# Kernel optimization log

Hardware: AMD Instinct MI355X
Metric: run time of the kernel (lower is better)

## Reference

```python
import jax, jax.numpy as jnp
import numpy as np

K = 16        # top-K nodes per sample (from self.K)
C_IN = 2048   # conv1 in_channels
C_OUT = 256   # conv1 out_channels
D_OUT = 512   # fc1 out_features (in_features = K*C_OUT = 4096)


def setup_inputs() -> dict:
    key = jax.random.key(0)
    k0, k1, k2 = jax.random.split(key, 3)
    N, W, H = 128, 16, 16
    sounds = jax.random.normal(k0, (N, C_IN, W, H), dtype=jnp.float32)
    conv_w = jax.random.normal(k1, (C_OUT, C_IN), dtype=jnp.float32) * 0.02
    conv_b = jnp.zeros((C_OUT,), jnp.float32)
    fc_w = jax.random.normal(k2, (D_OUT, K * C_OUT), dtype=jnp.float32) * 0.02
    fc_b = jnp.zeros((D_OUT,), jnp.float32)
    return {"sounds": sounds, "conv_w": conv_w, "conv_b": conv_b,
            "fc_w": fc_w, "fc_b": fc_b}


def _dynamic_lnorm(rows, cols):
    """Symmetric-normalized spatial-affinity graph over the K nodes.

    Reconstructs the (undefined) Graph_Init.Dynamic_Lnorm: adjacency from
    spatial proximity of node coordinates, D^{-1/2} A D^{-1/2}.
    rows, cols: [N, K] int -> Lnorm [N, K, K] float.
    """
    coords = jnp.stack([rows, cols], axis=-1).astype(jnp.float32)  # [N,K,2]
    d2 = jnp.sum((coords[:, :, None, :] - coords[:, None, :, :]) ** 2, axis=-1)
    A = jnp.exp(-d2 / (2.0 * K))          # soft adjacency, self-loop weight 1
    dinv = jax.lax.rsqrt(jnp.sum(A, axis=-1))
    return A * dinv[:, :, None] * dinv[:, None, :]


def reference(sounds, conv_w, conv_b, fc_w, fc_b):
    N, C, W, H = sounds.shape
    # channel-sum saliency map (the original adds all channels into Fre)
    fre = jnp.sum(sounds, axis=1)                       # [N, W, H]
    feat = fre.reshape(N, W * H)
    _, idx = jax.lax.top_k(feat, K)                     # [N, K] descending (== sort[:, :K])
    # faithful replication of the original (off-by-one) coordinate math
    rows = jnp.where(idx < H, idx // H, idx // H - 1)   # [N, K]
    cols = jnp.where(idx % H == 0, H - 1, idx % H - 1)  # [N, K]
    # gather node features: [N, K, C]
    nodes = sounds[jnp.arange(N)[:, None], :, rows, cols]
    lnorm = _dynamic_lnorm(rows, cols)                  # [N, K, K]
    # conv1x1 on [K, C, 1, 1] == per-node linear 2048 -> 256, then ReLU
    x = jax.nn.relu(jnp.einsum('nkc,oc->nko', nodes, conv_w) + conv_b)  # [N,K,256]
    # graph aggregation: Lnorm @ x per sample
    y = jnp.einsum('nij,njo->nio', lnorm, x)            # [N, K, 256]
    # flatten nodes and apply fc1 (4096 -> 512)
    return y.reshape(N, K * C_OUT) @ fc_w.T + fc_b      # [N, 512]
```

## Files before the change

### kernel.cpp

```cpp
#include <hip/hip_runtime.h>
#include <math.h>

typedef __attribute__((ext_vector_type(8))) short short8;
typedef __attribute__((ext_vector_type(4))) float f32x4;
typedef unsigned short ushort;
typedef unsigned int uint;

#define NB   128
#define CIN  2048
#define PP   256
#define KK   16
#define CO   256
#define DO   512

#define WS_PARTIAL 0
#define WS_POS     1048576
#define WS_LNORM   1050624
#define WS_NODES   1083392
#define WS_WB      3180544
#define WS_XPART   3442688
#define WS_Y       4491264

__device__ __forceinline__ ushort f2bf(float f) {
    uint u = __builtin_bit_cast(uint, f);
    u += 0x7fffu + ((u >> 16) & 1u);
    return (ushort)(u >> 16);
}

__global__ __launch_bounds__(256) void k_prep(const float* __restrict__ conv_w,
                                              ushort* __restrict__ Wb,
                                              const float* __restrict__ fcb,
                                              float* __restrict__ out) {
    int b = blockIdx.x, t = threadIdx.x;
    if (b < 512) {
        int idx = (b * 256 + t) * 4;
        float4 v = *(const float4*)(conv_w + idx);
        uint2 u;
        u.x = (uint)f2bf(v.x) | ((uint)f2bf(v.y) << 16);
        u.y = (uint)f2bf(v.z) | ((uint)f2bf(v.w) << 16);
        *(uint2*)(Wb + idx) = u;
    } else {
        int i = (b - 512) * 256 + t;
        out[i] = fcb[i & 511];
    }
}

__global__ __launch_bounds__(256) void k_reduce(const float* __restrict__ snd,
                                                float* __restrict__ partial) {
    int n = blockIdx.x, chunk = blockIdx.y, t = threadIdx.x;
    int sub = t >> 6, p4 = t & 63;
    const float4* base = (const float4*)(snd + (size_t)n * CIN * PP
                                         + (size_t)(chunk * 256 + sub * 64) * PP) + p4;
    float4 acc = make_float4(0.f, 0.f, 0.f, 0.f);
#pragma unroll 4
    for (int c = 0; c < 64; ++c) {
        float4 v = base[c * 64];
        acc.x += v.x; acc.y += v.y; acc.z += v.z; acc.w += v.w;
    }
    ((float4*)(partial + (size_t)(n * 32 + chunk * 4 + sub) * 256))[p4] = acc;
}

__global__ __launch_bounds__(256) void k_topk_lnorm(const float* __restrict__ partial,
                                                    int* __restrict__ pos,
                                                    float* __restrict__ lnorm) {
    int n = blockIdx.x, t = threadIdx.x;
    int lane = t & 63, wv = t >> 6;
    __shared__ float wval[4];
    __shared__ int   widx[4];
    __shared__ int   sel[16];
    __shared__ float rr[16], cc[16], dinv[16];
    __shared__ float Ash[256];

    float v = 0.f;
#pragma unroll 8
    for (int j = 0; j < 32; ++j) v += partial[(size_t)(n * 32 + j) * 256 + t];

    for (int k = 0; k < 16; ++k) {
        float bv = v; int bi = t;
#pragma unroll
        for (int off = 32; off > 0; off >>= 1) {
            float ov = __shfl_xor(bv, off, 64);
            int   oi = __shfl_xor(bi, off, 64);
            if (ov > bv || (ov == bv && oi < bi)) { bv = ov; bi = oi; }
        }
        if (lane == 0) { wval[wv] = bv; widx[wv] = bi; }
        __syncthreads();
        float best = wval[0]; int besti = widx[0];
#pragma unroll
        for (int w = 1; w < 4; ++w) {
            float ww = wval[w]; int wi = widx[w];
            if (ww > best || (ww == best && wi < besti)) { best = ww; besti = wi; }
        }
        if (t == besti) v = -INFINITY;
        if (t == 0) sel[k] = besti;
        __syncthreads();
    }

    if (t < 16) {
        int idx = sel[t];
        int r = (idx < 16) ? (idx >> 4) : ((idx >> 4) - 1);
        int c = ((idx & 15) == 0) ? 15 : ((idx & 15) - 1);
        pos[n * 16 + t] = r * 16 + c;
        rr[t] = (float)r; cc[t] = (float)c;
    }
    __syncthreads();
    {
        int i = t >> 4, j = t & 15;
        float dr = rr[i] - rr[j], dc = cc[i] - cc[j];
        Ash[t] = expf(-(dr * dr + dc * dc) * (1.0f / 32.0f));
    }
    __syncthreads();
    if (t < 16) {
        float srow = 0.f;
#pragma unroll
        for (int j = 0; j < 16; ++j) srow += Ash[t * 16 + j];
        dinv[t] = rsqrtf(srow);
    }
    __syncthreads();
    {
        int i = t >> 4, j = t & 15;
        lnorm[(size_t)n * 256 + t] = Ash[t] * dinv[i] * dinv[j];
    }
}

__global__ __launch_bounds__(256) void k_gather(const float* __restrict__ snd,
                                                const int* __restrict__ pos,
                                                ushort* __restrict__ nodes) {
    int n = blockIdx.x, cb = blockIdx.y, t = threadIdx.x;
    __shared__ int lpos[16];
    if (t < 16) lpos[t] = pos[n * 16 + t];
    __syncthreads();
    int k = t & 15, ci = t >> 4;
    int p = lpos[k];
    const float* base = snd + (size_t)n * CIN * PP + (size_t)(cb * 128 + ci * 8) * PP + p;
    uint q[4];
#pragma unroll
    for (int i = 0; i < 4; ++i) {
        ushort a = f2bf(base[(size_t)(2 * i) * PP]);
        ushort b = f2bf(base[(size_t)(2 * i + 1) * PP]);
        q[i] = (uint)a | ((uint)b << 16);
    }
    uint4 qq = make_uint4(q[0], q[1], q[2], q[3]);
    *(uint4*)(nodes + (size_t)(n * 16 + k) * 2048 + cb * 128 + ci * 8) = qq;
}

__global__ __launch_bounds__(256) void k_conv(const ushort* __restrict__ nodes,
                                              const ushort* __restrict__ Wb,
                                              float* __restrict__ Xpart) {
    int bm = blockIdx.x, bo = blockIdx.y, kc = blockIdx.z, t = threadIdx.x;
    int w = t >> 6, l = t & 63;
    int lm = l & 15, quad = l >> 4;
    __shared__ ushort As[64 * 40];
    __shared__ ushort Bs[64 * 40];
    f32x4 acc[4] = {{0.f,0.f,0.f,0.f},{0.f,0.f,0.f,0.f},{0.f,0.f,0.f,0.f},{0.f,0.f,0.f,0.f}};
    int m0 = bm * 64, o0 = bo * 64;
    int row = t >> 2, seg = t & 3;
    const ushort* asrc = nodes + (size_t)(m0 + row) * 2048 + seg * 8;
    const ushort* bsrc = Wb + (size_t)(o0 + row) * 2048 + seg * 8;
    uint4* adst = (uint4*)(As + row * 40 + seg * 8);
    uint4* bdst = (uint4*)(Bs + row * 40 + seg * 8);
    const ushort* ard = As + (w * 16 + lm) * 40 + quad * 8;
    const ushort* brd = Bs + lm * 40 + quad * 8;

    for (int c0 = kc * 1024; c0 < kc * 1024 + 1024; c0 += 32) {
        *adst = *(const uint4*)(asrc + c0);
        *bdst = *(const uint4*)(bsrc + c0);
        __syncthreads();
        short8 af = *(const short8*)ard;
#pragma unroll
        for (int ot = 0; ot < 4; ++ot) {
            short8 bf = *(const short8*)(brd + ot * 16 * 40);
            acc[ot] = __builtin_amdgcn_mfma_f32_16x16x32_bf16(af, bf, acc[ot], 0, 0, 0);
        }
        __syncthreads();
    }

    float* Xp = Xpart + (size_t)kc * 524288;
#pragma unroll
    for (int ot = 0; ot < 4; ++ot) {
        int o = o0 + ot * 16 + lm;
#pragma unroll
        for (int r = 0; r < 4; ++r) {
            int m = m0 + w * 16 + quad * 4 + r;
            Xp[(size_t)m * 256 + o] = acc[ot][r];
        }
    }
}

__global__ __launch_bounds__(256) void k_xmix(const float* __restrict__ Xpart,
                                              const float* __restrict__ bias,
                                              const float* __restrict__ lnorm,
                                              float* __restrict__ Y) {
    int n = blockIdx.x, o = threadIdx.x;
    __shared__ float ln[256];
    ln[o] = lnorm[(size_t)n * 256 + o];
    float b = bias[o];
    __syncthreads();
    float xv[16];
#pragma unroll
    for (int j = 0; j < 16; ++j) {
        size_t off = (size_t)(n * 16 + j) * 256 + o;
        xv[j] = fmaxf(Xpart[off] + Xpart[524288 + off] + b, 0.0f);
    }
#pragma unroll
    for (int i = 0; i < 16; ++i) {
        float a = 0.f;
#pragma unroll
        for (int j = 0; j < 16; ++j) a += ln[i * 16 + j] * xv[j];
        Y[(size_t)n * 4096 + i * 256 + o] = a;
    }
}

__global__ __launch_bounds__(256) void k_fc(const float* __restrict__ Y,
                                            const float* __restrict__ Fw,
                                            float* __restrict__ out) {
    int bn = blockIdx.x, bd = blockIdx.y, bk = blockIdx.z, t = threadIdx.x;
    int to = t & 15, tm = t >> 4;
    __shared__ float Ys[16 * 34];
    __shared__ float Fs[16 * 68];
    float acc[2][4] = {};
    int n0 = bn * 32, d0 = bd * 64, kbase = bk * 512;
    for (int c0 = kbase; c0 < kbase + 512; c0 += 16) {
#pragma unroll
        for (int i = 0; i < 2; ++i) {
            int e = i * 256 + t;
            int m = e >> 4, k = e & 15;
            Ys[k * 34 + m] = Y[(size_t)(n0 + m) * 4096 + c0 + k];
        }
#pragma unroll
        for (int i = 0; i < 4; ++i) {
            int e = i * 256 + t;
            int d = e >> 4, k = e & 15;
            Fs[k * 68 + d] = Fw[(size_t)(d0 + d) * 4096 + c0 + k];
        }
        __syncthreads();
#pragma unroll
        for (int k = 0; k < 16; ++k) {
            float2 a = *(const float2*)&Ys[k * 34 + tm * 2];
            float4 b = *(const float4*)&Fs[k * 68 + to * 4];
            acc[0][0] += a.x * b.x; acc[0][1] += a.x * b.y;
            acc[0][2] += a.x * b.z; acc[0][3] += a.x * b.w;
            acc[1][0] += a.y * b.x; acc[1][1] += a.y * b.y;
            acc[1][2] += a.y * b.z; acc[1][3] += a.y * b.w;
        }
        __syncthreads();
    }
#pragma unroll
    for (int i = 0; i < 2; ++i) {
        int nn = n0 + tm * 2 + i;
#pragma unroll
        for (int j = 0; j < 4; ++j) {
            int d = d0 + to * 4 + j;
            atomicAdd(&out[(size_t)nn * 512 + d], acc[i][j]);
        }
    }
}

extern "C" void kernel_launch(void* const* d_in, const int* in_sizes, int n_in,
                              void* d_out, int out_size, void* d_ws, size_t ws_size,
                              hipStream_t stream) {
    const float* snd    = (const float*)d_in[0];
    const float* conv_w = (const float*)d_in[1];
    const float* conv_b = (const float*)d_in[2];
    const float* fc_w   = (const float*)d_in[3];
    const float* fc_b   = (const float*)d_in[4];
    float* out = (float*)d_out;
    float* ws  = (float*)d_ws;

    float*  partial = ws + WS_PARTIAL;
    int*    pos     = (int*)(ws + WS_POS);
    float*  lnorm   = ws + WS_LNORM;
    ushort* nodes   = (ushort*)(ws + WS_NODES);
    ushort* Wb      = (ushort*)(ws + WS_WB);
    float*  Xpart   = ws + WS_XPART;
    float*  Y       = ws + WS_Y;

    k_prep<<<768, 256, 0, stream>>>(conv_w, Wb, fc_b, out);
    k_reduce<<<dim3(128, 8), 256, 0, stream>>>(snd, partial);
    k_topk_lnorm<<<128, 256, 0, stream>>>(partial, pos, lnorm);
    k_gather<<<dim3(128, 16), 256, 0, stream>>>(snd, pos, nodes);
    k_conv<<<dim3(32, 4, 2), 256, 0, stream>>>(nodes, Wb, Xpart);
    k_xmix<<<128, 256, 0, stream>>>(Xpart, conv_b, lnorm, Y);
    k_fc<<<dim3(4, 8, 8), 256, 0, stream>>>(Y, fc_w, out);
}
```

Measured before the change: 486.8 us.

## Coalesce node gather via wave shuffles and deepen split-K for conv and fc

The gather kernel now loads whole channel rows with coalesced float4 reads and picks the top-K positions with cross-lane shuffles, staging bf16 values in shared memory before packed writes. This replaces the scattered strided scalar loads. The conv kernel uses a 64-wide K tile with 8-way split-K for more blocks, and the channel-mix kernel sums 8 partials. The fc split-K doubles to 16. In exchange, the gather reads all spatial positions of each channel, and the extra partial buffers add memory traffic.

```diff
diff --git a/kernel.cpp b/kernel.cpp
--- a/kernel.cpp
+++ b/kernel.cpp
@@ -19,7 +19,7 @@
 #define WS_NODES   1083392
 #define WS_WB      3180544
 #define WS_XPART   3442688
-#define WS_Y       4491264
+#define WS_Y       7636992
 
 __device__ __forceinline__ ushort f2bf(float f) {
     uint u = __builtin_bit_cast(uint, f);
@@ -126,22 +126,38 @@
 __global__ __launch_bounds__(256) void k_gather(const float* __restrict__ snd,
                                                 const int* __restrict__ pos,
                                                 ushort* __restrict__ nodes) {
-    int n = blockIdx.x, cb = blockIdx.y, t = threadIdx.x;
+    int n = blockIdx.x, cg = blockIdx.y, t = threadIdx.x;
+    int w = t >> 6, l = t & 63;
     __shared__ int lpos[16];
+    __shared__ ushort Nsh[16][34];
     if (t < 16) lpos[t] = pos[n * 16 + t];
     __syncthreads();
-    int k = t & 15, ci = t >> 4;
-    int p = lpos[k];
-    const float* base = snd + (size_t)n * CIN * PP + (size_t)(cb * 128 + ci * 8) * PP + p;
-    uint q[4];
-#pragma unroll
-    for (int i = 0; i < 4; ++i) {
-        ushort a = f2bf(base[(size_t)(2 * i) * PP]);
-        ushort b = f2bf(base[(size_t)(2 * i + 1) * PP]);
-        q[i] = (uint)a | ((uint)b << 16);
-    }
-    uint4 qq = make_uint4(q[0], q[1], q[2], q[3]);
-    *(uint4*)(nodes + (size_t)(n * 16 + k) * 2048 + cb * 128 + ci * 8) = qq;
+
+    int p = lpos[l & 15];
+    int srclane = p >> 2;
+    int comp = p & 3;
+
+    const float4* rowbase = (const float4*)(snd + (size_t)n * CIN * PP
+                                            + (size_t)(cg * 32 + w * 8) * PP);
+    float4 vv[8];
+#pragma unroll
+    for (int cc = 0; cc < 8; ++cc) vv[cc] = rowbase[(size_t)cc * 64 + l];
+
+#pragma unroll
+    for (int cc = 0; cc < 8; ++cc) {
+        float s0 = __shfl(vv[cc].x, srclane, 64);
+        float s1 = __shfl(vv[cc].y, srclane, 64);
+        float s2 = __shfl(vv[cc].z, srclane, 64);
+        float s3 = __shfl(vv[cc].w, srclane, 64);
+        float val = (comp & 2) ? ((comp & 1) ? s3 : s2)
+                               : ((comp & 1) ? s1 : s0);
+        if (l < 16) Nsh[l][w * 8 + cc] = f2bf(val);
+    }
+    __syncthreads();
+
+    int kk = t >> 4, u = t & 15;
+    uint pv = (uint)Nsh[kk][u * 2] | ((uint)Nsh[kk][u * 2 + 1] << 16);
+    ((uint*)(nodes + (size_t)(n * 16 + kk) * 2048 + cg * 32))[u] = pv;
 }
 
 __global__ __launch_bounds__(256) void k_conv(const ushort* __restrict__ nodes,
@@ -150,27 +166,32 @@
     int bm = blockIdx.x, bo = blockIdx.y, kc = blockIdx.z, t = threadIdx.x;
     int w = t >> 6, l = t & 63;
     int lm = l & 15, quad = l >> 4;
-    __shared__ ushort As[64 * 40];
-    __shared__ ushort Bs[64 * 40];
+    __shared__ ushort As[64 * 72];
+    __shared__ ushort Bs[64 * 72];
     f32x4 acc[4] = {{0.f,0.f,0.f,0.f},{0.f,0.f,0.f,0.f},{0.f,0.f,0.f,0.f},{0.f,0.f,0.f,0.f}};
     int m0 = bm * 64, o0 = bo * 64;
-    int row = t >> 2, seg = t & 3;
-    const ushort* asrc = nodes + (size_t)(m0 + row) * 2048 + seg * 8;
-    const ushort* bsrc = Wb + (size_t)(o0 + row) * 2048 + seg * 8;
-    uint4* adst = (uint4*)(As + row * 40 + seg * 8);
-    uint4* bdst = (uint4*)(Bs + row * 40 + seg * 8);
-    const ushort* ard = As + (w * 16 + lm) * 40 + quad * 8;
-    const ushort* brd = Bs + lm * 40 + quad * 8;
-
-    for (int c0 = kc * 1024; c0 < kc * 1024 + 1024; c0 += 32) {
-        *adst = *(const uint4*)(asrc + c0);
-        *bdst = *(const uint4*)(bsrc + c0);
-        __syncthreads();
-        short8 af = *(const short8*)ard;
-#pragma unroll
-        for (int ot = 0; ot < 4; ++ot) {
-            short8 bf = *(const short8*)(brd + ot * 16 * 40);
-            acc[ot] = __builtin_amdgcn_mfma_f32_16x16x32_bf16(af, bf, acc[ot], 0, 0, 0);
+    int srow = t >> 3, seg = t & 7;
+    const ushort* ard = As + (w * 16 + lm) * 72 + quad * 8;
+    const ushort* brd = Bs + lm * 72 + quad * 8;
+
+    for (int c0 = kc * 256; c0 < kc * 256 + 256; c0 += 64) {
+#pragma unroll
+        for (int i = 0; i < 2; ++i) {
+            int r = i * 32 + srow;
+            *(uint4*)(As + r * 72 + seg * 8) =
+                *(const uint4*)(nodes + (size_t)(m0 + r) * 2048 + c0 + seg * 8);
+            *(uint4*)(Bs + r * 72 + seg * 8) =
+                *(const uint4*)(Wb + (size_t)(o0 + r) * 2048 + c0 + seg * 8);
+        }
+        __syncthreads();
+#pragma unroll
+        for (int ks = 0; ks < 2; ++ks) {
+            short8 af = *(const short8*)(ard + ks * 32);
+#pragma unroll
+            for (int ot = 0; ot < 4; ++ot) {
+                short8 bf = *(const short8*)(brd + ot * 16 * 72 + ks * 32);
+                acc[ot] = __builtin_amdgcn_mfma_f32_16x16x32_bf16(af, bf, acc[ot], 0, 0, 0);
+            }
         }
         __syncthreads();
     }
@@ -200,7 +221,10 @@
 #pragma unroll
     for (int j = 0; j < 16; ++j) {
         size_t off = (size_t)(n * 16 + j) * 256 + o;
-        xv[j] = fmaxf(Xpart[off] + Xpart[524288 + off] + b, 0.0f);
+        float s = b;
+#pragma unroll
+        for (int kc = 0; kc < 8; ++kc) s += Xpart[(size_t)kc * 524288 + off];
+        xv[j] = fmaxf(s, 0.0f);
     }
 #pragma unroll
     for (int i = 0; i < 16; ++i) {
@@ -219,8 +243,8 @@
     __shared__ float Ys[16 * 34];
     __shared__ float Fs[16 * 68];
     float acc[2][4] = {};
-    int n0 = bn * 32, d0 = bd * 64, kbase = bk * 512;
-    for (int c0 = kbase; c0 < kbase + 512; c0 += 16) {
+    int n0 = bn * 32, d0 = bd * 64, kbase = bk * 256;
+    for (int c0 = kbase; c0 < kbase + 256; c0 += 16) {
 #pragma unroll
         for (int i = 0; i < 2; ++i) {
             int e = i * 256 + t;
@@ -278,8 +302,8 @@
     k_prep<<<768, 256, 0, stream>>>(conv_w, Wb, fc_b, out);
     k_reduce<<<dim3(128, 8), 256, 0, stream>>>(snd, partial);
     k_topk_lnorm<<<128, 256, 0, stream>>>(partial, pos, lnorm);
-    k_gather<<<dim3(128, 16), 256, 0, stream>>>(snd, pos, nodes);
-    k_conv<<<dim3(32, 4, 2), 256, 0, stream>>>(nodes, Wb, Xpart);
+    k_gather<<<dim3(128, 64), 256, 0, stream>>>(snd, pos, nodes);
+    k_conv<<<dim3(32, 4, 8), 256, 0, stream>>>(nodes, Wb, Xpart);
     k_xmix<<<128, 256, 0, stream>>>(Xpart, conv_b, lnorm, Y);
-    k_fc<<<dim3(4, 8, 8), 256, 0, stream>>>(Y, fc_w, out);
-}
+    k_fc<<<dim3(4, 8, 16), 256, 0, stream>>>(Y, fc_w, out);
+}
```

Measured after the change: 474.4 us. 2.5% less time.
